# Performance work log

Hardware: AMD Instinct MI355X
Metric: run time of the kernel (lower is better)

Reference implementation:

```python
import jax, jax.numpy as jnp
import numpy as np

HEADS = 8  # from init_kwargs

def setup_inputs() -> dict:
    key = jax.random.key(0)
    ks = jax.random.split(key, 9)
    N, S, E = 8, 2048, 512
    scale = 1.0 / np.sqrt(E)
    return {
        "values": jax.random.normal(ks[0], (N, S, E), jnp.float32),
        "keys": jax.random.normal(ks[1], (N, S, E), jnp.float32),
        "query": jax.random.normal(ks[2], (N, S, E), jnp.float32),
        "mask": jnp.ones((N, 1, 1, S), jnp.int32),
        "Wv": jax.random.normal(ks[3], (E, E), jnp.float32) * scale,
        "Wk": jax.random.normal(ks[4], (E, E), jnp.float32) * scale,
        "Wq": jax.random.normal(ks[5], (E, E), jnp.float32) * scale,
        "Wo": jax.random.normal(ks[6], (E, E), jnp.float32) * scale,
        "bo": jnp.zeros((E,), jnp.float32),
    }

def reference(values, keys, query, mask, Wv, Wk, Wq, Wo, bo):
    N, Q, E = query.shape
    H = HEADS
    D = E // H
    v = (values @ Wv).reshape(N, -1, H, D)  # [N,K,H,D]
    k = (keys @ Wk).reshape(N, -1, H, D)
    q = (query @ Wq).reshape(N, Q, H, D)
    energy = jnp.einsum('nqhd,nkhd->nhqk', q, k)  # [N,H,Q,K]
    energy = jnp.where(mask == 0, jnp.float32(-1e20), energy)
    attn = jax.nn.softmax(energy / jnp.sqrt(jnp.float32(D)), axis=3)
    out = jnp.einsum('nhqk,nkhd->nqhd', attn, v).reshape(N, Q, E)
    return out @ Wo + bo
```

## Files before the change

### kernel.cpp

```cpp
#include <hip/hip_runtime.h>
#include <hip/hip_bf16.h>
#include <stdint.h>

typedef __bf16 bf16;
typedef __bf16 bf16x8 __attribute__((ext_vector_type(8)));
typedef __bf16 bf16x4v __attribute__((ext_vector_type(4)));
typedef float  f32x4  __attribute__((ext_vector_type(4)));
typedef float  f32x16 __attribute__((ext_vector_type(16)));
typedef unsigned int u32x4 __attribute__((ext_vector_type(4)));

#define NB    8
#define SEQ   2048
#define EMB   512
#define NHEAD 8
#define HD    64

static __device__ __forceinline__ f32x4 mfma16(bf16x8 a, bf16x8 b, f32x4 c) {
    return __builtin_amdgcn_mfma_f32_16x16x32_bf16(a, b, c, 0, 0, 0);
}
static __device__ __forceinline__ f32x16 mfma32(bf16x8 a, bf16x8 b, f32x16 c) {
    return __builtin_amdgcn_mfma_f32_32x32x16_bf16(a, b, c, 0, 0, 0);
}
static __device__ __forceinline__ float ex2(float x) {
    float r; asm("v_exp_f32 %0, %1" : "=v"(r) : "v"(x)); return r;
}
static __device__ __forceinline__ unsigned pkbf(float lo, float hi) {
    unsigned d; asm("v_cvt_pk_bf16_f32 %0, %1, %2" : "=v"(d) : "v"(lo), "v"(hi)); return d;
}
static __device__ __forceinline__ float max3(float a, float b, float c) {
    return fmaxf(fmaxf(a, b), c);
}
static __device__ __forceinline__ void gload_lds16(const void* g, void* l) {
    __builtin_amdgcn_global_load_lds(
        (const __attribute__((address_space(1))) unsigned int*)g,
        (__attribute__((address_space(3))) unsigned int*)l, 16, 0, 0);
}
#define PRIO1 __builtin_amdgcn_s_setprio(1)
#define PRIO0 __builtin_amdgcn_s_setprio(0)

__global__ __launch_bounds__(256) void prep_weights(
    const float* __restrict__ Wv, const float* __restrict__ Wk,
    const float* __restrict__ Wq, const float* __restrict__ Wo,
    bf16* __restrict__ wt)
{
    int idx = blockIdx.x * 256 + threadIdx.x;
    int w   = idx >> 18;
    int rem = idx & 262143;
    int k   = rem >> 9;
    int n   = rem & 511;
    const float* src = (w == 0) ? Wv : (w == 1) ? Wk : (w == 2) ? Wq : Wo;
    wt[(size_t)w * 262144 + (size_t)n * 512 + k] = (bf16)src[k * 512 + n];
}

template <bool A_F32, bool FINAL>
__global__ __launch_bounds__(256) void gemm_kernel(
    const void* __restrict__ Ap, const bf16* __restrict__ Bt,
    void* __restrict__ Cp, const float* __restrict__ bias)
{
    __shared__ __align__(16) bf16 As[128][72];
    __shared__ __align__(16) bf16 Bs[128][72];

    const int t    = threadIdx.x;
    const int lane = t & 63;
    const int wave = t >> 6;
    const int wr   = wave >> 1, wc = wave & 1;
    const int l15  = lane & 15, lg = lane >> 4;
    const long row0 = (long)blockIdx.x * 128;
    const int  col0 = blockIdx.y * 128;

    f32x4 acc[4][4];
#pragma unroll
    for (int i = 0; i < 4; i++)
#pragma unroll
        for (int j = 0; j < 4; j++) acc[i][j] = (f32x4){0.f, 0.f, 0.f, 0.f};

    for (int k0 = 0; k0 < 512; k0 += 64) {
        __syncthreads();
        if (A_F32) {
            const float* A = (const float*)Ap;
#pragma unroll
            for (int i = 0; i < 8; i++) {
                int c  = t + 256 * i;
                int r  = c >> 4;
                int cc = (c & 15) * 4;
                f32x4 v = *(const f32x4*)(A + (row0 + r) * 512 + k0 + cc);
                bf16x4v pk = { (bf16)v[0], (bf16)v[1], (bf16)v[2], (bf16)v[3] };
                *(bf16x4v*)&As[r][cc] = pk;
            }
        } else {
            const bf16* A = (const bf16*)Ap;
#pragma unroll
            for (int i = 0; i < 4; i++) {
                int c  = t + 256 * i;
                int r  = c >> 3;
                int cc = (c & 7) * 8;
                *(bf16x8*)&As[r][cc] = *(const bf16x8*)(A + (row0 + r) * 512 + k0 + cc);
            }
        }
#pragma unroll
        for (int i = 0; i < 4; i++) {
            int c  = t + 256 * i;
            int r  = c >> 3;
            int cc = (c & 7) * 8;
            *(bf16x8*)&Bs[r][cc] = *(const bf16x8*)(Bt + (size_t)(col0 + r) * 512 + k0 + cc);
        }
        __syncthreads();
#pragma unroll
        for (int kc = 0; kc < 64; kc += 32) {
            bf16x8 af[4], bfv[4];
#pragma unroll
            for (int mb = 0; mb < 4; mb++)
                af[mb] = *(bf16x8*)&As[wr * 64 + mb * 16 + l15][kc + lg * 8];
#pragma unroll
            for (int nb = 0; nb < 4; nb++)
                bfv[nb] = *(bf16x8*)&Bs[wc * 64 + nb * 16 + l15][kc + lg * 8];
#pragma unroll
            for (int mb = 0; mb < 4; mb++)
#pragma unroll
                for (int nb = 0; nb < 4; nb++)
                    acc[mb][nb] = mfma16(af[mb], bfv[nb], acc[mb][nb]);
        }
    }

#pragma unroll
    for (int mb = 0; mb < 4; mb++)
#pragma unroll
        for (int nb = 0; nb < 4; nb++)
#pragma unroll
            for (int r = 0; r < 4; r++) {
                long grow = row0 + wr * 64 + mb * 16 + lg * 4 + r;
                int  gcol = col0 + wc * 64 + nb * 16 + l15;
                float v = acc[mb][nb][r];
                if (FINAL) {
                    ((float*)Cp)[grow * 512 + gcol] = v + bias[gcol];
                } else {
                    ((bf16*)Cp)[grow * 512 + gcol] = (bf16)v;
                }
            }
}

__global__ __launch_bounds__(512, 2) void attn_kernel(
    const bf16* __restrict__ Qg, const bf16* __restrict__ Kg,
    const bf16* __restrict__ Vg, const int* __restrict__ mask,
    bf16* __restrict__ ctx)
{
    __shared__ __align__(16) bf16 Ks[4][4096];
    __shared__ __align__(16) bf16 Vt[4][4096];
    __shared__ __align__(16) bf16 Ob[8][32 * 72];

    const int t    = threadIdx.x;
    const int lane = t & 63;
    const int w    = t >> 6;
    const int l31  = lane & 31;
    const int hi   = lane >> 5;
    const int qt = blockIdx.x, h = blockIdx.y, n = blockIdx.z;

    const size_t nbase   = (size_t)n * SEQ;
    const size_t headoff = (size_t)h * 64;
    const int q0 = qt * 512 + w * 64;

    int* mflags = (int*)&Ob[0][0];
    {
        const int* mp0 = mask + n * SEQ + t * 4;
        int mok = (mp0[0] != 0) & (mp0[1] != 0) & (mp0[2] != 0) & (mp0[3] != 0);
        unsigned long long b = __ballot(mok);
        if (lane == 0) mflags[w] = (b == ~0ULL) ? 1 : 0;
    }

    bf16x8 qf[2][4];
#pragma unroll
    for (int qb = 0; qb < 2; ++qb)
#pragma unroll
        for (int ds = 0; ds < 4; ++ds)
            qf[qb][ds] = *(const bf16x8*)(Qg + (nbase + q0 + qb * 32 + l31) * 512 + headoff + ds * 16 + hi * 8);

    f32x16 o[2][2] = {};
    float m_run[2] = {-1e30f, -1e30f};
    float l_run[2] = {0.f, 0.f};

    const bf16* kg = Kg + (nbase + w * 8 + (lane >> 3)) * 512 + headoff + (((lane & 7) ^ (lane >> 3)) << 3);
    const bf16* vg = Vg + (nbase + lane) * 512 + headoff + w * 8;
    const int*  mp = mask + n * SEQ;

#define VSCAT(VR, VB) do {                                                    \
        char* vbp = (char*)(VB);                                              \
        _Pragma("unroll") for (int j = 0; j < 8; ++j)                         \
            *(bf16*)(vbp + (8 * w + j) * 128 + ((2 * lane) ^ (j << 4))) = (VR)[j]; \
    } while (0)

    gload_lds16(kg,                     (char*)&Ks[0][0] + w * 1024);
    gload_lds16(kg + (size_t)64 * 512,  (char*)&Ks[1][0] + w * 1024);
    bf16x8 vrA = *(const bf16x8*)vg;
    bf16x8 vrB = *(const bf16x8*)(vg + (size_t)64 * 512);
    VSCAT(vrA, &Vt[0][0]);
    VSCAT(vrB, &Vt[1][0]);
    __syncthreads();
    const int maskall = mflags[0] & mflags[1] & mflags[2] & mflags[3] &
                        mflags[4] & mflags[5] & mflags[6] & mflags[7];

    const float SC = 0.18033688011f;

    f32x16 p[2][2];
    u32x4  bq[2][4];

#define QK_TILE(KB) do {                                                      \
        const char* kbb = (const char*)(KB);                                  \
        f32x16 zz = {};                                                       \
        p[0][0] = zz; p[0][1] = zz; p[1][0] = zz; p[1][1] = zz;               \
        PRIO1;                                                                \
        _Pragma("unroll")                                                     \
        for (int ds = 0; ds < 4; ++ds) {                                      \
            int sw = (ds * 32 + hi * 16) ^ ((l31 & 7) << 4);                  \
            bf16x8 kf0 = *(const bf16x8*)(kbb + l31 * 128 + sw);              \
            bf16x8 kf1 = *(const bf16x8*)(kbb + (32 + l31) * 128 + sw);       \
            p[0][0] = mfma32(kf0, qf[0][ds], p[0][0]);                        \
            p[1][0] = mfma32(kf0, qf[1][ds], p[1][0]);                        \
            p[0][1] = mfma32(kf1, qf[0][ds], p[0][1]);                        \
            p[1][1] = mfma32(kf1, qf[1][ds], p[1][1]);                        \
        }                                                                     \
        PRIO0;                                                                \
    } while (0)

#define MASK_TILE(T) do {                                                     \
        if (!maskall) {                                                       \
            int mv = mp[(T) * 64 + lane];                                     \
            unsigned long long mb = __ballot(mv != 0);                        \
            if (mb != ~0ULL) {                                                \
                _Pragma("unroll") for (int qb = 0; qb < 2; ++qb)              \
                _Pragma("unroll") for (int kb = 0; kb < 2; ++kb) {            \
                    float* pp = (float*)&p[qb][kb];                           \
                    _Pragma("unroll") for (int r = 0; r < 16; ++r) {          \
                        int kk = kb * 32 + (r & 3) + 8 * (r >> 2) + 4 * hi;   \
                        if (!((mb >> kk) & 1)) pp[r] = -1e30f;                \
                    }                                                         \
                }                                                             \
            }                                                                 \
        }                                                                     \
    } while (0)

#define SM_PACK do {                                                          \
        _Pragma("unroll")                                                     \
        for (int qb = 0; qb < 2; ++qb) {                                      \
            float* p0 = (float*)&p[qb][0];                                    \
            float* p1 = (float*)&p[qb][1];                                    \
            float g0 = max3(p0[0], p0[1], p0[2]);                             \
            float g1 = max3(p0[3], p0[4], p0[5]);                             \
            float g2 = max3(p0[6], p0[7], p0[8]);                             \
            float g3 = max3(p0[9], p0[10], p0[11]);                           \
            float g4 = max3(p0[12], p0[13], p0[14]);                          \
            float g5 = max3(p0[15], p1[0], p1[1]);                            \
            float g6 = max3(p1[2], p1[3], p1[4]);                             \
            float g7 = max3(p1[5], p1[6], p1[7]);                             \
            float g8 = max3(p1[8], p1[9], p1[10]);                            \
            float g9 = max3(p1[11], p1[12], p1[13]);                          \
            float g10 = fmaxf(p1[14], p1[15]);                                \
            float t0 = max3(g0, g1, g2), t1 = max3(g3, g4, g5);               \
            float t2 = max3(g6, g7, g8), t3 = max3(g9, g10, t0);              \
            float tm = max3(t1, t2, t3);                                      \
            float tms = tm * SC;                                              \
            float rmax = fmaxf(tms, __shfl_xor(tms, 32));                     \
            if (!__all(rmax <= m_run[qb] + 8.0f)) {                           \
                float mn  = fmaxf(m_run[qb], rmax);                           \
                float fac = ex2(m_run[qb] - mn);                              \
                _Pragma("unroll") for (int db = 0; db < 2; ++db) {            \
                    float* oo = (float*)&o[db][qb];                           \
                    _Pragma("unroll") for (int r = 0; r < 16; ++r) oo[r] *= fac; \
                }                                                             \
                l_run[qb] *= fac; m_run[qb] = mn;                             \
            }                                                                 \
            float negm = -m_run[qb];                                          \
            float sa0 = 0.f, sa1 = 0.f, sa2 = 0.f, sa3 = 0.f;                 \
            _Pragma("unroll") for (int r = 0; r < 16; r += 4) {               \
                float e0 = ex2(fmaf(p0[r],   SC, negm)); p0[r]   = e0; sa0 += e0; \
                float e1 = ex2(fmaf(p0[r+1], SC, negm)); p0[r+1] = e1; sa1 += e1; \
                float e2 = ex2(fmaf(p0[r+2], SC, negm)); p0[r+2] = e2; sa2 += e2; \
                float e3 = ex2(fmaf(p0[r+3], SC, negm)); p0[r+3] = e3; sa3 += e3; \
            }                                                                 \
            _Pragma("unroll") for (int r = 0; r < 16; r += 4) {               \
                float e0 = ex2(fmaf(p1[r],   SC, negm)); p1[r]   = e0; sa0 += e0; \
                float e1 = ex2(fmaf(p1[r+1], SC, negm)); p1[r+1] = e1; sa1 += e1; \
                float e2 = ex2(fmaf(p1[r+2], SC, negm)); p1[r+2] = e2; sa2 += e2; \
                float e3 = ex2(fmaf(p1[r+3], SC, negm)); p1[r+3] = e3; sa3 += e3; \
            }                                                                 \
            float sl = (sa0 + sa1) + (sa2 + sa3);                             \
            l_run[qb] += sl + __shfl_xor(sl, 32);                             \
            _Pragma("unroll")                                                 \
            for (int ks = 0; ks < 4; ++ks) {                                  \
                float* ps = (ks >> 1) ? p1 : p0;                              \
                int bo = (ks & 1) * 8;                                        \
                unsigned A  = pkbf(ps[bo + 0], ps[bo + 1]);                   \
                unsigned B  = pkbf(ps[bo + 2], ps[bo + 3]);                   \
                unsigned C  = pkbf(ps[bo + 4], ps[bo + 5]);                   \
                unsigned Dw = pkbf(ps[bo + 6], ps[bo + 7]);                   \
                unsigned xA = __shfl_xor(A, 32), xB = __shfl_xor(B, 32);      \
                unsigned xC = __shfl_xor(C, 32), xD = __shfl_xor(Dw, 32);     \
                unsigned w0 = hi ? xC : A, w1 = hi ? xD : B;                  \
                unsigned w2 = hi ? C : xA, w3 = hi ? Dw : xB;                 \
                bq[qb][ks] = (u32x4){w0, w1, w2, w3};                         \
            }                                                                 \
        }                                                                     \
    } while (0)

#define PV_TILE(VB) do {                                                      \
        const char* vbb = (const char*)(VB);                                  \
        PRIO1;                                                                \
        _Pragma("unroll")                                                     \
        for (int ks = 0; ks < 4; ++ks) {                                      \
            int sw = (ks * 32 + hi * 16) ^ ((l31 & 7) << 4);                  \
            bf16x8 vf0 = *(const bf16x8*)(vbb + l31 * 128 + sw);              \
            bf16x8 vf1 = *(const bf16x8*)(vbb + (32 + l31) * 128 + sw);       \
            union { u32x4 u; bf16x8 v; } c0, c1;                              \
            c0.u = bq[0][ks]; c1.u = bq[1][ks];                               \
            o[0][0] = mfma32(vf0, c0.v, o[0][0]);                             \
            o[0][1] = mfma32(vf0, c1.v, o[0][1]);                             \
            o[1][0] = mfma32(vf1, c0.v, o[1][0]);                             \
            o[1][1] = mfma32(vf1, c1.v, o[1][1]);                             \
        }                                                                     \
        PRIO0;                                                                \
    } while (0)

    u32x4 bqA[2][4];

    for (int e = 0; e < 16; ++e) {
        const int bA = (e & 1) * 2, bB = bA + 1;
        const int nA = bA ^ 2,      nB = bB ^ 2;
        if (e < 15) {
            gload_lds16(kg + (size_t)(2 * e + 2) * 64 * 512, (char*)&Ks[nA][0] + w * 1024);
            gload_lds16(kg + (size_t)(2 * e + 3) * 64 * 512, (char*)&Ks[nB][0] + w * 1024);
            vrA = *(const bf16x8*)(vg + (size_t)(2 * e + 2) * 64 * 512);
            vrB = *(const bf16x8*)(vg + (size_t)(2 * e + 3) * 64 * 512);
        }
        QK_TILE(&Ks[bA][0]);
        MASK_TILE(2 * e);
        SM_PACK;
#pragma unroll
        for (int qb = 0; qb < 2; ++qb)
#pragma unroll
            for (int ks = 0; ks < 4; ++ks) bqA[qb][ks] = bq[qb][ks];
        QK_TILE(&Ks[bB][0]);
        PV_TILE(&Vt[bA][0]);
#pragma unroll
        for (int qb = 0; qb < 2; ++qb)
#pragma unroll
            for (int ks = 0; ks < 4; ++ks) bq[qb][ks] = bqA[qb][ks];
        MASK_TILE(2 * e + 1);
        SM_PACK;
        PV_TILE(&Vt[bB][0]);
        if (e < 15) {
            VSCAT(vrA, &Vt[nA][0]);
            VSCAT(vrB, &Vt[nB][0]);
        }
        __syncthreads();
    }

#pragma unroll
    for (int qb = 0; qb < 2; ++qb) {
        float inv = 1.f / l_run[qb];
        bf16* ob = &Ob[w][0];
#pragma unroll
        for (int db = 0; db < 2; ++db) {
            float* oo = (float*)&o[db][qb];
#pragma unroll
            for (int r = 0; r < 16; ++r) {
                int d = db * 32 + (r & 3) + 8 * (r >> 2) + 4 * hi;
                ob[l31 * 72 + d] = (bf16)(oo[r] * inv);
            }
        }
#pragma unroll
        for (int i = 0; i < 2; ++i)
#pragma unroll
            for (int half = 0; half < 2; ++half) {
                int ql = i * 16 + (lane >> 2);
                int d8 = (lane & 3) * 8 + half * 32;
                bf16x8 vv = *(const bf16x8*)(ob + ql * 72 + d8);
                *(bf16x8*)(ctx + (nbase + q0 + qb * 32 + ql) * 512 + headoff + d8) = vv;
            }
    }
#undef VSCAT
#undef QK_TILE
#undef MASK_TILE
#undef SM_PACK
#undef PV_TILE
}

extern "C" void kernel_launch(void* const* d_in, const int* in_sizes, int n_in,
                              void* d_out, int out_size, void* d_ws, size_t ws_size,
                              hipStream_t stream) {
    (void)in_sizes; (void)n_in; (void)out_size; (void)ws_size;
    const float* values = (const float*)d_in[0];
    const float* keys   = (const float*)d_in[1];
    const float* query  = (const float*)d_in[2];
    const int*   mask   = (const int*)d_in[3];
    const float* Wv = (const float*)d_in[4];
    const float* Wk = (const float*)d_in[5];
    const float* Wq = (const float*)d_in[6];
    const float* Wo = (const float*)d_in[7];
    const float* bo = (const float*)d_in[8];
    float* out = (float*)d_out;

    char* ws = (char*)d_ws;
    bf16* wt = (bf16*)(ws);
    bf16* Qb = (bf16*)(ws + ((size_t)2  << 20));
    bf16* Kb = (bf16*)(ws + ((size_t)18 << 20));
    bf16* Vb = (bf16*)(ws + ((size_t)34 << 20));
    bf16* Cb = (bf16*)(ws + ((size_t)50 << 20));

    prep_weights<<<4096, 256, 0, stream>>>(Wv, Wk, Wq, Wo, wt);
    gemm_kernel<true, false><<<dim3(128, 4), 256, 0, stream>>>(values, wt,              Vb, nullptr);
    gemm_kernel<true, false><<<dim3(128, 4), 256, 0, stream>>>(keys,   wt + 262144,     Kb, nullptr);
    gemm_kernel<true, false><<<dim3(128, 4), 256, 0, stream>>>(query,  wt + 2 * 262144, Qb, nullptr);
    attn_kernel<<<dim3(4, 8, 8), 512, 0, stream>>>(Qb, Kb, Vb, mask, Cb);
    gemm_kernel<false, true><<<dim3(128, 4), 256, 0, stream>>>(Cb, wt + 3 * 262144, out, bo);
}
```

Before: 179.8 us.

## Split attention work across 16 waves of 32 query rows each

The attention block grows from 512 to 1024 threads, so each wave now handles 32 query rows instead of 64. This halves the per-wave Q fragments, score tiles and output accumulators. The K/V tile loads are split so each half of the waves fetches one of the two 64-key tiles, and the buffers move into a single shared LDS array. The old interleaving of QK for the next tile with PV for the previous one is dropped in favour of a simple sequential order. The aim is to put more waves on each CU to hide latency, at the cost of less instruction-level overlap per wave and possible register pressure from the launch bounds of 1024 threads with 4 blocks.

```diff
diff --git a/kernel.cpp b/kernel.cpp
--- a/kernel.cpp
+++ b/kernel.cpp
@@ -139,84 +139,79 @@
             }
 }
 
-__global__ __launch_bounds__(512, 2) void attn_kernel(
+__global__ __launch_bounds__(1024, 4) void attn_kernel(
     const bf16* __restrict__ Qg, const bf16* __restrict__ Kg,
     const bf16* __restrict__ Vg, const int* __restrict__ mask,
     bf16* __restrict__ ctx)
 {
-    __shared__ __align__(16) bf16 Ks[4][4096];
-    __shared__ __align__(16) bf16 Vt[4][4096];
-    __shared__ __align__(16) bf16 Ob[8][32 * 72];
+    __shared__ __align__(16) char smem[73792];
+    int* mflags = (int*)(smem + 73728);
 
     const int t    = threadIdx.x;
     const int lane = t & 63;
     const int w    = t >> 6;
+    const int wA   = w & 7;
+    const int wT   = w >> 3;
     const int l31  = lane & 31;
     const int hi   = lane >> 5;
     const int qt = blockIdx.x, h = blockIdx.y, n = blockIdx.z;
 
     const size_t nbase   = (size_t)n * SEQ;
     const size_t headoff = (size_t)h * 64;
-    const int q0 = qt * 512 + w * 64;
-
-    int* mflags = (int*)&Ob[0][0];
+    const int q0 = qt * 512 + w * 32;
+
     {
-        const int* mp0 = mask + n * SEQ + t * 4;
-        int mok = (mp0[0] != 0) & (mp0[1] != 0) & (mp0[2] != 0) & (mp0[3] != 0);
+        const int* mp0 = mask + n * SEQ + t * 2;
+        int mok = (mp0[0] != 0) & (mp0[1] != 0);
         unsigned long long b = __ballot(mok);
         if (lane == 0) mflags[w] = (b == ~0ULL) ? 1 : 0;
     }
 
-    bf16x8 qf[2][4];
-#pragma unroll
-    for (int qb = 0; qb < 2; ++qb)
-#pragma unroll
-        for (int ds = 0; ds < 4; ++ds)
-            qf[qb][ds] = *(const bf16x8*)(Qg + (nbase + q0 + qb * 32 + l31) * 512 + headoff + ds * 16 + hi * 8);
-
-    f32x16 o[2][2] = {};
-    float m_run[2] = {-1e30f, -1e30f};
-    float l_run[2] = {0.f, 0.f};
-
-    const bf16* kg = Kg + (nbase + w * 8 + (lane >> 3)) * 512 + headoff + (((lane & 7) ^ (lane >> 3)) << 3);
-    const bf16* vg = Vg + (nbase + lane) * 512 + headoff + w * 8;
+    bf16x8 qf[4];
+#pragma unroll
+    for (int ds = 0; ds < 4; ++ds)
+        qf[ds] = *(const bf16x8*)(Qg + (nbase + q0 + l31) * 512 + headoff + ds * 16 + hi * 8);
+
+    f32x16 o[2] = {};
+    float m_run = -1e30f;
+    float l_run = 0.f;
+
+    const bf16* kg = Kg + (nbase + wA * 8 + (lane >> 3)) * 512 + headoff + (((lane & 7) ^ (lane >> 3)) << 3);
+    const bf16* vg = Vg + (nbase + lane) * 512 + headoff + wA * 8;
     const int*  mp = mask + n * SEQ;
 
-#define VSCAT(VR, VB) do {                                                    \
-        char* vbp = (char*)(VB);                                              \
+#define VSCAT(VR, BUF) do {                                                   \
+        char* vbp = smem + 32768 + (BUF) * 8192;                              \
         _Pragma("unroll") for (int j = 0; j < 8; ++j)                         \
-            *(bf16*)(vbp + (8 * w + j) * 128 + ((2 * lane) ^ (j << 4))) = (VR)[j]; \
-    } while (0)
-
-    gload_lds16(kg,                     (char*)&Ks[0][0] + w * 1024);
-    gload_lds16(kg + (size_t)64 * 512,  (char*)&Ks[1][0] + w * 1024);
-    bf16x8 vrA = *(const bf16x8*)vg;
-    bf16x8 vrB = *(const bf16x8*)(vg + (size_t)64 * 512);
-    VSCAT(vrA, &Vt[0][0]);
-    VSCAT(vrB, &Vt[1][0]);
+            *(bf16*)(vbp + (8 * wA + j) * 128 + ((2 * lane) ^ (j << 4))) = (VR)[j]; \
+    } while (0)
+
+    bf16x8 vr;
+    gload_lds16(kg + (size_t)wT * 64 * 512, smem + wT * 8192 + wA * 1024);
+    vr = *(const bf16x8*)(vg + (size_t)wT * 64 * 512);
+    VSCAT(vr, wT);
     __syncthreads();
-    const int maskall = mflags[0] & mflags[1] & mflags[2] & mflags[3] &
-                        mflags[4] & mflags[5] & mflags[6] & mflags[7];
+    int maskall = 1;
+#pragma unroll
+    for (int i = 0; i < 16; ++i) maskall &= mflags[i];
 
     const float SC = 0.18033688011f;
 
-    f32x16 p[2][2];
-    u32x4  bq[2][4];
-
-#define QK_TILE(KB) do {                                                      \
-        const char* kbb = (const char*)(KB);                                  \
+    f32x16 p[2];
+    u32x4  bq[4];
+
+#define QK_TILE(BUF) do {                                                     \
+        const char* kbb = smem + (BUF) * 8192;                                \
         f32x16 zz = {};                                                       \
-        p[0][0] = zz; p[0][1] = zz; p[1][0] = zz; p[1][1] = zz;               \
+        p[0] = zz; p[1] = zz;                                                 \
         PRIO1;                                                                \
         _Pragma("unroll")                                                     \
         for (int ds = 0; ds < 4; ++ds) {                                      \
             int sw = (ds * 32 + hi * 16) ^ ((l31 & 7) << 4);                  \
             bf16x8 kf0 = *(const bf16x8*)(kbb + l31 * 128 + sw);              \
             bf16x8 kf1 = *(const bf16x8*)(kbb + (32 + l31) * 128 + sw);       \
-            p[0][0] = mfma32(kf0, qf[0][ds], p[0][0]);                        \
-            p[1][0] = mfma32(kf0, qf[1][ds], p[1][0]);                        \
-            p[0][1] = mfma32(kf1, qf[0][ds], p[0][1]);                        \
-            p[1][1] = mfma32(kf1, qf[1][ds], p[1][1]);                        \
+            p[0] = mfma32(kf0, qf[ds], p[0]);                                 \
+            p[1] = mfma32(kf1, qf[ds], p[1]);                                 \
         }                                                                     \
         PRIO0;                                                                \
     } while (0)
@@ -226,9 +221,8 @@
             int mv = mp[(T) * 64 + lane];                                     \
             unsigned long long mb = __ballot(mv != 0);                        \
             if (mb != ~0ULL) {                                                \
-                _Pragma("unroll") for (int qb = 0; qb < 2; ++qb)              \
                 _Pragma("unroll") for (int kb = 0; kb < 2; ++kb) {            \
-                    float* pp = (float*)&p[qb][kb];                           \
+                    float* pp = (float*)&p[kb];                               \
                     _Pragma("unroll") for (int r = 0; r < 16; ++r) {          \
                         int kk = kb * 32 + (r & 3) + 8 * (r >> 2) + 4 * hi;   \
                         if (!((mb >> kk) & 1)) pp[r] = -1e30f;                \
@@ -239,127 +233,106 @@
     } while (0)
 
 #define SM_PACK do {                                                          \
+        float* p0 = (float*)&p[0];                                            \
+        float* p1 = (float*)&p[1];                                            \
+        float g0 = max3(p0[0], p0[1], p0[2]);                                 \
+        float g1 = max3(p0[3], p0[4], p0[5]);                                 \
+        float g2 = max3(p0[6], p0[7], p0[8]);                                 \
+        float g3 = max3(p0[9], p0[10], p0[11]);                               \
+        float g4 = max3(p0[12], p0[13], p0[14]);                              \
+        float g5 = max3(p0[15], p1[0], p1[1]);                                \
+        float g6 = max3(p1[2], p1[3], p1[4]);                                 \
+        float g7 = max3(p1[5], p1[6], p1[7]);                                 \
+        float g8 = max3(p1[8], p1[9], p1[10]);                                \
+        float g9 = max3(p1[11], p1[12], p1[13]);                              \
+        float g10 = fmaxf(p1[14], p1[15]);                                    \
+        float t0 = max3(g0, g1, g2), t1 = max3(g3, g4, g5);                   \
+        float t2 = max3(g6, g7, g8), t3 = max3(g9, g10, t0);                  \
+        float tm = max3(t1, t2, t3);                                          \
+        float tms = tm * SC;                                                  \
+        float rmax = fmaxf(tms, __shfl_xor(tms, 32));                         \
+        if (!__all(rmax <= m_run + 8.0f)) {                                   \
+            float mn  = fmaxf(m_run, rmax);                                   \
+            float fac = ex2(m_run - mn);                                      \
+            _Pragma("unroll") for (int db = 0; db < 2; ++db) {                \
+                float* oo = (float*)&o[db];                                   \
+                _Pragma("unroll") for (int r = 0; r < 16; ++r) oo[r] *= fac;  \
+            }                                                                 \
+            l_run *= fac; m_run = mn;                                         \
+        }                                                                     \
+        float negm = -m_run;                                                  \
+        float sa0 = 0.f, sa1 = 0.f, sa2 = 0.f, sa3 = 0.f;                     \
+        _Pragma("unroll") for (int r = 0; r < 16; r += 4) {                   \
+            float e0 = ex2(fmaf(p0[r],   SC, negm)); p0[r]   = e0; sa0 += e0; \
+            float e1 = ex2(fmaf(p0[r+1], SC, negm)); p0[r+1] = e1; sa1 += e1; \
+            float e2 = ex2(fmaf(p0[r+2], SC, negm)); p0[r+2] = e2; sa2 += e2; \
+            float e3 = ex2(fmaf(p0[r+3], SC, negm)); p0[r+3] = e3; sa3 += e3; \
+        }                                                                     \
+        _Pragma("unroll") for (int r = 0; r < 16; r += 4) {                   \
+            float e0 = ex2(fmaf(p1[r],   SC, negm)); p1[r]   = e0; sa0 += e0; \
+            float e1 = ex2(fmaf(p1[r+1], SC, negm)); p1[r+1] = e1; sa1 += e1; \
+            float e2 = ex2(fmaf(p1[r+2], SC, negm)); p1[r+2] = e2; sa2 += e2; \
+            float e3 = ex2(fmaf(p1[r+3], SC, negm)); p1[r+3] = e3; sa3 += e3; \
+        }                                                                     \
+        float sl = (sa0 + sa1) + (sa2 + sa3);                                 \
+        l_run += sl + __shfl_xor(sl, 32);                                     \
         _Pragma("unroll")                                                     \
-        for (int qb = 0; qb < 2; ++qb) {                                      \
-            float* p0 = (float*)&p[qb][0];                                    \
-            float* p1 = (float*)&p[qb][1];                                    \
-            float g0 = max3(p0[0], p0[1], p0[2]);                             \
-            float g1 = max3(p0[3], p0[4], p0[5]);                             \
-            float g2 = max3(p0[6], p0[7], p0[8]);                             \
-            float g3 = max3(p0[9], p0[10], p0[11]);                           \
-            float g4 = max3(p0[12], p0[13], p0[14]);                          \
-            float g5 = max3(p0[15], p1[0], p1[1]);                            \
-            float g6 = max3(p1[2], p1[3], p1[4]);                             \
-            float g7 = max3(p1[5], p1[6], p1[7]);                             \
-            float g8 = max3(p1[8], p1[9], p1[10]);                            \
-            float g9 = max3(p1[11], p1[12], p1[13]);                          \
-            float g10 = fmaxf(p1[14], p1[15]);                                \
-            float t0 = max3(g0, g1, g2), t1 = max3(g3, g4, g5);               \
-            float t2 = max3(g6, g7, g8), t3 = max3(g9, g10, t0);              \
-            float tm = max3(t1, t2, t3);                                      \
-            float tms = tm * SC;                                              \
-            float rmax = fmaxf(tms, __shfl_xor(tms, 32));                     \
-            if (!__all(rmax <= m_run[qb] + 8.0f)) {                           \
-                float mn  = fmaxf(m_run[qb], rmax);                           \
-                float fac = ex2(m_run[qb] - mn);                              \
-                _Pragma("unroll") for (int db = 0; db < 2; ++db) {            \
-                    float* oo = (float*)&o[db][qb];                           \
-                    _Pragma("unroll") for (int r = 0; r < 16; ++r) oo[r] *= fac; \
-                }                                                             \
-                l_run[qb] *= fac; m_run[qb] = mn;                             \
-            }                                                                 \
-            float negm = -m_run[qb];                                          \
-            float sa0 = 0.f, sa1 = 0.f, sa2 = 0.f, sa3 = 0.f;                 \
-            _Pragma("unroll") for (int r = 0; r < 16; r += 4) {               \
-                float e0 = ex2(fmaf(p0[r],   SC, negm)); p0[r]   = e0; sa0 += e0; \
-                float e1 = ex2(fmaf(p0[r+1], SC, negm)); p0[r+1] = e1; sa1 += e1; \
-                float e2 = ex2(fmaf(p0[r+2], SC, negm)); p0[r+2] = e2; sa2 += e2; \
-                float e3 = ex2(fmaf(p0[r+3], SC, negm)); p0[r+3] = e3; sa3 += e3; \
-            }                                                                 \
-            _Pragma("unroll") for (int r = 0; r < 16; r += 4) {               \
-                float e0 = ex2(fmaf(p1[r],   SC, negm)); p1[r]   = e0; sa0 += e0; \
-                float e1 = ex2(fmaf(p1[r+1], SC, negm)); p1[r+1] = e1; sa1 += e1; \
-                float e2 = ex2(fmaf(p1[r+2], SC, negm)); p1[r+2] = e2; sa2 += e2; \
-                float e3 = ex2(fmaf(p1[r+3], SC, negm)); p1[r+3] = e3; sa3 += e3; \
-            }                                                                 \
-            float sl = (sa0 + sa1) + (sa2 + sa3);                             \
-            l_run[qb] += sl + __shfl_xor(sl, 32);                             \
-            _Pragma("unroll")                                                 \
-            for (int ks = 0; ks < 4; ++ks) {                                  \
-                float* ps = (ks >> 1) ? p1 : p0;                              \
-                int bo = (ks & 1) * 8;                                        \
-                unsigned A  = pkbf(ps[bo + 0], ps[bo + 1]);                   \
-                unsigned B  = pkbf(ps[bo + 2], ps[bo + 3]);                   \
-                unsigned C  = pkbf(ps[bo + 4], ps[bo + 5]);                   \
-                unsigned Dw = pkbf(ps[bo + 6], ps[bo + 7]);                   \
-                unsigned xA = __shfl_xor(A, 32), xB = __shfl_xor(B, 32);      \
-                unsigned xC = __shfl_xor(C, 32), xD = __shfl_xor(Dw, 32);     \
-                unsigned w0 = hi ? xC : A, w1 = hi ? xD : B;                  \
-                unsigned w2 = hi ? C : xA, w3 = hi ? Dw : xB;                 \
-                bq[qb][ks] = (u32x4){w0, w1, w2, w3};                         \
-            }                                                                 \
-        }                                                                     \
-    } while (0)
-
-#define PV_TILE(VB) do {                                                      \
-        const char* vbb = (const char*)(VB);                                  \
+        for (int ks = 0; ks < 4; ++ks) {                                      \
+            float* ps = (ks >> 1) ? p1 : p0;                                  \
+            int bo = (ks & 1) * 8;                                            \
+            unsigned A  = pkbf(ps[bo + 0], ps[bo + 1]);                       \
+            unsigned B  = pkbf(ps[bo + 2], ps[bo + 3]);                       \
+            unsigned C  = pkbf(ps[bo + 4], ps[bo + 5]);                       \
+            unsigned Dw = pkbf(ps[bo + 6], ps[bo + 7]);                       \
+            unsigned xA = __shfl_xor(A, 32), xB = __shfl_xor(B, 32);          \
+            unsigned xC = __shfl_xor(C, 32), xD = __shfl_xor(Dw, 32);         \
+            unsigned w0 = hi ? xC : A, w1 = hi ? xD : B;                      \
+            unsigned w2 = hi ? C : xA, w3 = hi ? Dw : xB;                     \
+            bq[ks] = (u32x4){w0, w1, w2, w3};                                 \
+        }                                                                     \
+    } while (0)
+
+#define PV_TILE(BUF) do {                                                     \
+        const char* vbb = smem + 32768 + (BUF) * 8192;                        \
         PRIO1;                                                                \
         _Pragma("unroll")                                                     \
         for (int ks = 0; ks < 4; ++ks) {                                      \
             int sw = (ks * 32 + hi * 16) ^ ((l31 & 7) << 4);                  \
             bf16x8 vf0 = *(const bf16x8*)(vbb + l31 * 128 + sw);              \
             bf16x8 vf1 = *(const bf16x8*)(vbb + (32 + l31) * 128 + sw);       \
-            union { u32x4 u; bf16x8 v; } c0, c1;                              \
-            c0.u = bq[0][ks]; c1.u = bq[1][ks];                               \
-            o[0][0] = mfma32(vf0, c0.v, o[0][0]);                             \
-            o[0][1] = mfma32(vf0, c1.v, o[0][1]);                             \
-            o[1][0] = mfma32(vf1, c0.v, o[1][0]);                             \
-            o[1][1] = mfma32(vf1, c1.v, o[1][1]);                             \
+            union { u32x4 u; bf16x8 v; } c0;                                  \
+            c0.u = bq[ks];                                                    \
+            o[0] = mfma32(vf0, c0.v, o[0]);                                   \
+            o[1] = mfma32(vf1, c0.v, o[1]);                                   \
         }                                                                     \
         PRIO0;                                                                \
     } while (0)
-
-    u32x4 bqA[2][4];
 
     for (int e = 0; e < 16; ++e) {
         const int bA = (e & 1) * 2, bB = bA + 1;
-        const int nA = bA ^ 2,      nB = bB ^ 2;
         if (e < 15) {
-            gload_lds16(kg + (size_t)(2 * e + 2) * 64 * 512, (char*)&Ks[nA][0] + w * 1024);
-            gload_lds16(kg + (size_t)(2 * e + 3) * 64 * 512, (char*)&Ks[nB][0] + w * 1024);
-            vrA = *(const bf16x8*)(vg + (size_t)(2 * e + 2) * 64 * 512);
-            vrB = *(const bf16x8*)(vg + (size_t)(2 * e + 3) * 64 * 512);
-        }
-        QK_TILE(&Ks[bA][0]);
+            gload_lds16(kg + (size_t)(2 * e + 2 + wT) * 64 * 512,
+                        smem + ((bA ^ 2) + wT) * 8192 + wA * 1024);
+            vr = *(const bf16x8*)(vg + (size_t)(2 * e + 2 + wT) * 64 * 512);
+        }
+        QK_TILE(bA);
         MASK_TILE(2 * e);
         SM_PACK;
-#pragma unroll
-        for (int qb = 0; qb < 2; ++qb)
-#pragma unroll
-            for (int ks = 0; ks < 4; ++ks) bqA[qb][ks] = bq[qb][ks];
-        QK_TILE(&Ks[bB][0]);
-        PV_TILE(&Vt[bA][0]);
-#pragma unroll
-        for (int qb = 0; qb < 2; ++qb)
-#pragma unroll
-            for (int ks = 0; ks < 4; ++ks) bq[qb][ks] = bqA[qb][ks];
+        PV_TILE(bA);
+        QK_TILE(bB);
         MASK_TILE(2 * e + 1);
         SM_PACK;
-        PV_TILE(&Vt[bB][0]);
-        if (e < 15) {
-            VSCAT(vrA, &Vt[nA][0]);
-            VSCAT(vrB, &Vt[nB][0]);
-        }
+        PV_TILE(bB);
+        if (e < 15) VSCAT(vr, (bA ^ 2) + wT);
         __syncthreads();
     }
 
-#pragma unroll
-    for (int qb = 0; qb < 2; ++qb) {
-        float inv = 1.f / l_run[qb];
-        bf16* ob = &Ob[w][0];
+    {
+        float inv = 1.f / l_run;
+        bf16* ob = (bf16*)(smem + w * 4608);
 #pragma unroll
         for (int db = 0; db < 2; ++db) {
-            float* oo = (float*)&o[db][qb];
+            float* oo = (float*)&o[db];
 #pragma unroll
             for (int r = 0; r < 16; ++r) {
                 int d = db * 32 + (r & 3) + 8 * (r >> 2) + 4 * hi;
@@ -373,7 +346,7 @@
                 int ql = i * 16 + (lane >> 2);
                 int d8 = (lane & 3) * 8 + half * 32;
                 bf16x8 vv = *(const bf16x8*)(ob + ql * 72 + d8);
-                *(bf16x8*)(ctx + (nbase + q0 + qb * 32 + ql) * 512 + headoff + d8) = vv;
+                *(bf16x8*)(ctx + (nbase + q0 + ql) * 512 + headoff + d8) = vv;
             }
     }
 #undef VSCAT
@@ -409,6 +382,6 @@
     gemm_kernel<true, false><<<dim3(128, 4), 256, 0, stream>>>(values, wt,              Vb, nullptr);
     gemm_kernel<true, false><<<dim3(128, 4), 256, 0, stream>>>(keys,   wt + 262144,     Kb, nullptr);
     gemm_kernel<true, false><<<dim3(128, 4), 256, 0, stream>>>(query,  wt + 2 * 262144, Qb, nullptr);
-    attn_kernel<<<dim3(4, 8, 8), 512, 0, stream>>>(Qb, Kb, Vb, mask, Cb);
+    attn_kernel<<<dim3(4, 8, 8), 1024, 0, stream>>>(Qb, Kb, Vb, mask, Cb);
     gemm_kernel<false, true><<<dim3(128, 4), 256, 0, stream>>>(Cb, wt + 3 * 262144, out, bo);
 }
```

Measured after the change: 218.3 us. +21.4%, slower.

## Pre-transpose V in projection GEMM and stream K/V from global into registers

Applied to the files above, without the earlier changes.

The V projection GEMM now writes its output transposed per head (d-major, key-contiguous) through an LDS staging tile. The attention kernel drops its LDS K/V double buffers, per-tile scatter-transpose and block barriers. Each wave instead loads its K and V MFMA fragments straight from global memory into registers, prefetching the next K tile while the current one computes. The grid order is also changed so that the head index varies fastest. This removes LDS traffic and synchronisation, but each wave now issues redundant global loads of the same K/V (8 waves per block read identical data), so the kernel relies on L2 and L1 caching and must hide global latency with only one tile of prefetch.

```diff
diff --git a/kernel.cpp b/kernel.cpp
--- a/kernel.cpp
+++ b/kernel.cpp
@@ -29,11 +29,6 @@
 }
 static __device__ __forceinline__ float max3(float a, float b, float c) {
     return fmaxf(fmaxf(a, b), c);
-}
-static __device__ __forceinline__ void gload_lds16(const void* g, void* l) {
-    __builtin_amdgcn_global_load_lds(
-        (const __attribute__((address_space(1))) unsigned int*)g,
-        (__attribute__((address_space(3))) unsigned int*)l, 16, 0, 0);
 }
 #define PRIO1 __builtin_amdgcn_s_setprio(1)
 #define PRIO0 __builtin_amdgcn_s_setprio(0)
@@ -52,7 +47,7 @@
     wt[(size_t)w * 262144 + (size_t)n * 512 + k] = (bf16)src[k * 512 + n];
 }
 
-template <bool A_F32, bool FINAL>
+template <bool A_F32, bool FINAL, bool VT>
 __global__ __launch_bounds__(256) void gemm_kernel(
     const void* __restrict__ Ap, const bf16* __restrict__ Bt,
     void* __restrict__ Cp, const float* __restrict__ bias)
@@ -122,50 +117,75 @@
         }
     }
 
-#pragma unroll
-    for (int mb = 0; mb < 4; mb++)
-#pragma unroll
-        for (int nb = 0; nb < 4; nb++)
-#pragma unroll
-            for (int r = 0; r < 4; r++) {
-                long grow = row0 + wr * 64 + mb * 16 + lg * 4 + r;
-                int  gcol = col0 + wc * 64 + nb * 16 + l15;
-                float v = acc[mb][nb][r];
-                if (FINAL) {
-                    ((float*)Cp)[grow * 512 + gcol] = v + bias[gcol];
-                } else {
-                    ((bf16*)Cp)[grow * 512 + gcol] = (bf16)v;
+    if constexpr (VT) {
+        __shared__ __align__(16) bf16 Cs[128][138];
+#pragma unroll
+        for (int mb = 0; mb < 4; mb++)
+#pragma unroll
+            for (int nb = 0; nb < 4; nb++)
+#pragma unroll
+                for (int r = 0; r < 4; r++) {
+                    int keyl = wr * 64 + mb * 16 + lg * 4 + r;
+                    int dl   = wc * 64 + nb * 16 + l15;
+                    Cs[dl][keyl] = (bf16)acc[mb][nb][r];
                 }
-            }
+        __syncthreads();
+        const int n_idx = (int)(row0 >> 11);
+        const int key0  = (int)(row0 & 2047);
+        const int dl    = t >> 1;
+        const int half  = t & 1;
+        bf16* dst = (bf16*)Cp + ((size_t)n_idx * 512 + col0 + dl) * 2048 + key0 + half * 64;
+#pragma unroll
+        for (int c = 0; c < 8; ++c)
+            *(bf16x8*)(dst + c * 8) = *(const bf16x8*)&Cs[dl][half * 64 + c * 8];
+    } else {
+#pragma unroll
+        for (int mb = 0; mb < 4; mb++)
+#pragma unroll
+            for (int nb = 0; nb < 4; nb++)
+#pragma unroll
+                for (int r = 0; r < 4; r++) {
+                    long grow = row0 + wr * 64 + mb * 16 + lg * 4 + r;
+                    int  gcol = col0 + wc * 64 + nb * 16 + l15;
+                    float v = acc[mb][nb][r];
+                    if (FINAL) {
+                        ((float*)Cp)[grow * 512 + gcol] = v + bias[gcol];
+                    } else {
+                        ((bf16*)Cp)[grow * 512 + gcol] = (bf16)v;
+                    }
+                }
+    }
 }
 
 __global__ __launch_bounds__(512, 2) void attn_kernel(
     const bf16* __restrict__ Qg, const bf16* __restrict__ Kg,
-    const bf16* __restrict__ Vg, const int* __restrict__ mask,
+    const bf16* __restrict__ Vtg, const int* __restrict__ maskp,
     bf16* __restrict__ ctx)
 {
-    __shared__ __align__(16) bf16 Ks[4][4096];
-    __shared__ __align__(16) bf16 Vt[4][4096];
     __shared__ __align__(16) bf16 Ob[8][32 * 72];
+    __shared__ int mflags[8];
 
     const int t    = threadIdx.x;
     const int lane = t & 63;
     const int w    = t >> 6;
     const int l31  = lane & 31;
     const int hi   = lane >> 5;
-    const int qt = blockIdx.x, h = blockIdx.y, n = blockIdx.z;
+    const int h = blockIdx.x, n = blockIdx.y, qt = blockIdx.z;
 
     const size_t nbase   = (size_t)n * SEQ;
     const size_t headoff = (size_t)h * 64;
     const int q0 = qt * 512 + w * 64;
 
-    int* mflags = (int*)&Ob[0][0];
     {
-        const int* mp0 = mask + n * SEQ + t * 4;
+        const int* mp0 = maskp + n * SEQ + t * 4;
         int mok = (mp0[0] != 0) & (mp0[1] != 0) & (mp0[2] != 0) & (mp0[3] != 0);
         unsigned long long b = __ballot(mok);
         if (lane == 0) mflags[w] = (b == ~0ULL) ? 1 : 0;
     }
+    __syncthreads();
+    int maskall = 1;
+#pragma unroll
+    for (int i = 0; i < 8; ++i) maskall &= mflags[i];
 
     bf16x8 qf[2][4];
 #pragma unroll
@@ -178,45 +198,39 @@
     float m_run[2] = {-1e30f, -1e30f};
     float l_run[2] = {0.f, 0.f};
 
-    const bf16* kg = Kg + (nbase + w * 8 + (lane >> 3)) * 512 + headoff + (((lane & 7) ^ (lane >> 3)) << 3);
-    const bf16* vg = Vg + (nbase + lane) * 512 + headoff + w * 8;
-    const int*  mp = mask + n * SEQ;
-
-#define VSCAT(VR, VB) do {                                                    \
-        char* vbp = (char*)(VB);                                              \
-        _Pragma("unroll") for (int j = 0; j < 8; ++j)                         \
-            *(bf16*)(vbp + (8 * w + j) * 128 + ((2 * lane) ^ (j << 4))) = (VR)[j]; \
-    } while (0)
-
-    gload_lds16(kg,                     (char*)&Ks[0][0] + w * 1024);
-    gload_lds16(kg + (size_t)64 * 512,  (char*)&Ks[1][0] + w * 1024);
-    bf16x8 vrA = *(const bf16x8*)vg;
-    bf16x8 vrB = *(const bf16x8*)(vg + (size_t)64 * 512);
-    VSCAT(vrA, &Vt[0][0]);
-    VSCAT(vrB, &Vt[1][0]);
-    __syncthreads();
-    const int maskall = mflags[0] & mflags[1] & mflags[2] & mflags[3] &
-                        mflags[4] & mflags[5] & mflags[6] & mflags[7];
+    const bf16* kb = Kg + nbase * 512 + headoff;
+    const bf16* vb = Vtg + ((size_t)n * 512 + h * 64) * 2048;
+    const int*  mp = maskp + n * SEQ;
 
     const float SC = 0.18033688011f;
 
     f32x16 p[2][2];
     u32x4  bq[2][4];
-
-#define QK_TILE(KB) do {                                                      \
-        const char* kbb = (const char*)(KB);                                  \
+    bf16x8 kf[2][4];
+    bf16x8 vf[2][4];
+
+#define KLOAD(KT) do {                                                        \
+        _Pragma("unroll") for (int kk = 0; kk < 2; ++kk)                      \
+        _Pragma("unroll") for (int ds = 0; ds < 4; ++ds)                      \
+            kf[kk][ds] = *(const bf16x8*)(kb + (size_t)((KT) * 64 + kk * 32 + l31) * 512 + ds * 16 + hi * 8); \
+    } while (0)
+
+#define VLOAD(KT) do {                                                        \
+        _Pragma("unroll") for (int dh = 0; dh < 2; ++dh)                      \
+        _Pragma("unroll") for (int ks = 0; ks < 4; ++ks)                      \
+            vf[dh][ks] = *(const bf16x8*)(vb + (size_t)(dh * 32 + l31) * 2048 + (KT) * 64 + ks * 16 + hi * 8); \
+    } while (0)
+
+#define QK_TILE do {                                                          \
         f32x16 zz = {};                                                       \
         p[0][0] = zz; p[0][1] = zz; p[1][0] = zz; p[1][1] = zz;               \
         PRIO1;                                                                \
         _Pragma("unroll")                                                     \
         for (int ds = 0; ds < 4; ++ds) {                                      \
-            int sw = (ds * 32 + hi * 16) ^ ((l31 & 7) << 4);                  \
-            bf16x8 kf0 = *(const bf16x8*)(kbb + l31 * 128 + sw);              \
-            bf16x8 kf1 = *(const bf16x8*)(kbb + (32 + l31) * 128 + sw);       \
-            p[0][0] = mfma32(kf0, qf[0][ds], p[0][0]);                        \
-            p[1][0] = mfma32(kf0, qf[1][ds], p[1][0]);                        \
-            p[0][1] = mfma32(kf1, qf[0][ds], p[0][1]);                        \
-            p[1][1] = mfma32(kf1, qf[1][ds], p[1][1]);                        \
+            p[0][0] = mfma32(kf[0][ds], qf[0][ds], p[0][0]);                  \
+            p[1][0] = mfma32(kf[0][ds], qf[1][ds], p[1][0]);                  \
+            p[0][1] = mfma32(kf[1][ds], qf[0][ds], p[0][1]);                  \
+            p[1][1] = mfma32(kf[1][ds], qf[1][ds], p[1][1]);                  \
         }                                                                     \
         PRIO0;                                                                \
     } while (0)
@@ -227,11 +241,11 @@
             unsigned long long mb = __ballot(mv != 0);                        \
             if (mb != ~0ULL) {                                                \
                 _Pragma("unroll") for (int qb = 0; qb < 2; ++qb)              \
-                _Pragma("unroll") for (int kb = 0; kb < 2; ++kb) {            \
-                    float* pp = (float*)&p[qb][kb];                           \
+                _Pragma("unroll") for (int kk = 0; kk < 2; ++kk) {            \
+                    float* pp = (float*)&p[qb][kk];                           \
                     _Pragma("unroll") for (int r = 0; r < 16; ++r) {          \
-                        int kk = kb * 32 + (r & 3) + 8 * (r >> 2) + 4 * hi;   \
-                        if (!((mb >> kk) & 1)) pp[r] = -1e30f;                \
+                        int kkk = kk * 32 + (r & 3) + 8 * (r >> 2) + 4 * hi;  \
+                        if (!((mb >> kkk) & 1)) pp[r] = -1e30f;               \
                     }                                                         \
                 }                                                             \
             }                                                                 \
@@ -301,56 +315,28 @@
         }                                                                     \
     } while (0)
 
-#define PV_TILE(VB) do {                                                      \
-        const char* vbb = (const char*)(VB);                                  \
+#define PV_TILE do {                                                          \
         PRIO1;                                                                \
         _Pragma("unroll")                                                     \
         for (int ks = 0; ks < 4; ++ks) {                                      \
-            int sw = (ks * 32 + hi * 16) ^ ((l31 & 7) << 4);                  \
-            bf16x8 vf0 = *(const bf16x8*)(vbb + l31 * 128 + sw);              \
-            bf16x8 vf1 = *(const bf16x8*)(vbb + (32 + l31) * 128 + sw);       \
             union { u32x4 u; bf16x8 v; } c0, c1;                              \
             c0.u = bq[0][ks]; c1.u = bq[1][ks];                               \
-            o[0][0] = mfma32(vf0, c0.v, o[0][0]);                             \
-            o[0][1] = mfma32(vf0, c1.v, o[0][1]);                             \
-            o[1][0] = mfma32(vf1, c0.v, o[1][0]);                             \
-            o[1][1] = mfma32(vf1, c1.v, o[1][1]);                             \
+            o[0][0] = mfma32(vf[0][ks], c0.v, o[0][0]);                       \
+            o[0][1] = mfma32(vf[0][ks], c1.v, o[0][1]);                       \
+            o[1][0] = mfma32(vf[1][ks], c0.v, o[1][0]);                       \
+            o[1][1] = mfma32(vf[1][ks], c1.v, o[1][1]);                       \
         }                                                                     \
         PRIO0;                                                                \
     } while (0)
 
-    u32x4 bqA[2][4];
-
-    for (int e = 0; e < 16; ++e) {
-        const int bA = (e & 1) * 2, bB = bA + 1;
-        const int nA = bA ^ 2,      nB = bB ^ 2;
-        if (e < 15) {
-            gload_lds16(kg + (size_t)(2 * e + 2) * 64 * 512, (char*)&Ks[nA][0] + w * 1024);
-            gload_lds16(kg + (size_t)(2 * e + 3) * 64 * 512, (char*)&Ks[nB][0] + w * 1024);
-            vrA = *(const bf16x8*)(vg + (size_t)(2 * e + 2) * 64 * 512);
-            vrB = *(const bf16x8*)(vg + (size_t)(2 * e + 3) * 64 * 512);
-        }
-        QK_TILE(&Ks[bA][0]);
-        MASK_TILE(2 * e);
+    KLOAD(0);
+    for (int kt = 0; kt < 32; ++kt) {
+        VLOAD(kt);
+        QK_TILE;
+        if (kt < 31) KLOAD(kt + 1);
+        MASK_TILE(kt);
         SM_PACK;
-#pragma unroll
-        for (int qb = 0; qb < 2; ++qb)
-#pragma unroll
-            for (int ks = 0; ks < 4; ++ks) bqA[qb][ks] = bq[qb][ks];
-        QK_TILE(&Ks[bB][0]);
-        PV_TILE(&Vt[bA][0]);
-#pragma unroll
-        for (int qb = 0; qb < 2; ++qb)
-#pragma unroll
-            for (int ks = 0; ks < 4; ++ks) bq[qb][ks] = bqA[qb][ks];
-        MASK_TILE(2 * e + 1);
-        SM_PACK;
-        PV_TILE(&Vt[bB][0]);
-        if (e < 15) {
-            VSCAT(vrA, &Vt[nA][0]);
-            VSCAT(vrB, &Vt[nB][0]);
-        }
-        __syncthreads();
+        PV_TILE;
     }
 
 #pragma unroll
@@ -376,7 +362,8 @@
                 *(bf16x8*)(ctx + (nbase + q0 + qb * 32 + ql) * 512 + headoff + d8) = vv;
             }
     }
-#undef VSCAT
+#undef KLOAD
+#undef VLOAD
 #undef QK_TILE
 #undef MASK_TILE
 #undef SM_PACK
@@ -399,16 +386,16 @@
     float* out = (float*)d_out;
 
     char* ws = (char*)d_ws;
-    bf16* wt = (bf16*)(ws);
-    bf16* Qb = (bf16*)(ws + ((size_t)2  << 20));
-    bf16* Kb = (bf16*)(ws + ((size_t)18 << 20));
-    bf16* Vb = (bf16*)(ws + ((size_t)34 << 20));
-    bf16* Cb = (bf16*)(ws + ((size_t)50 << 20));
+    bf16* wt  = (bf16*)(ws);
+    bf16* Qb  = (bf16*)(ws + ((size_t)2  << 20));
+    bf16* Kb  = (bf16*)(ws + ((size_t)18 << 20));
+    bf16* VbT = (bf16*)(ws + ((size_t)34 << 20));
+    bf16* Cb  = (bf16*)(ws + ((size_t)50 << 20));
 
     prep_weights<<<4096, 256, 0, stream>>>(Wv, Wk, Wq, Wo, wt);
-    gemm_kernel<true, false><<<dim3(128, 4), 256, 0, stream>>>(values, wt,              Vb, nullptr);
-    gemm_kernel<true, false><<<dim3(128, 4), 256, 0, stream>>>(keys,   wt + 262144,     Kb, nullptr);
-    gemm_kernel<true, false><<<dim3(128, 4), 256, 0, stream>>>(query,  wt + 2 * 262144, Qb, nullptr);
-    attn_kernel<<<dim3(4, 8, 8), 512, 0, stream>>>(Qb, Kb, Vb, mask, Cb);
-    gemm_kernel<false, true><<<dim3(128, 4), 256, 0, stream>>>(Cb, wt + 3 * 262144, out, bo);
-}
+    gemm_kernel<true, false, true ><<<dim3(128, 4), 256, 0, stream>>>(values, wt,              VbT, nullptr);
+    gemm_kernel<true, false, false><<<dim3(128, 4), 256, 0, stream>>>(keys,   wt + 262144,     Kb,  nullptr);
+    gemm_kernel<true, false, false><<<dim3(128, 4), 256, 0, stream>>>(query,  wt + 2 * 262144, Qb,  nullptr);
+    attn_kernel<<<dim3(8, 8, 4), 512, 0, stream>>>(Qb, Kb, VbT, mask, Cb);
+    gemm_kernel<false, true, false><<<dim3(128, 4), 256, 0, stream>>>(Cb, wt + 3 * 262144, out, bo);
+}
```

Measured after the change: 212.4 us. 18.1% more time.
